# Kernel tuning notes

Measured on AMD Instinct MI355X. Metric: run time of the kernel, lower is better.

Reference implementation:

```python
import jax, jax.numpy as jnp
import numpy as np

PI = 3.14159265358979323846
MARGIN = 6.0
DIM = 256
ENT_TOT = 43234
REL_RANGE = (6.0 + 2.0) / DIM  # (margin + epsilon) / dim = 0.03125


def setup_inputs() -> dict:
    key = jax.random.key(0)
    k1, k2, k3 = jax.random.split(key, 3)
    head = jax.random.normal(k1, (32, 2 * DIM), dtype=jnp.float32)
    relation = jax.random.normal(k2, (32, DIM), dtype=jnp.float32)
    ent_emb = jax.random.normal(k3, (ENT_TOT, 2 * DIM), dtype=jnp.float32)
    return {"head": head, "relation": relation, "ent_emb": ent_emb}


def reference(head, relation, ent_emb):
    # head: (B, 2D) -> re/im halves (B, D)
    re_h, im_h = jnp.split(head, 2, axis=-1)
    # entity table: (E, 2D) -> (E, D) each
    re_t, im_t = jnp.split(ent_emb, 2, axis=-1)
    # phase rotation from relation embedding
    phase = relation / (REL_RANGE / PI)          # (B, D)
    re_r = jnp.cos(phase)
    im_r = jnp.sin(phase)
    # complex rotation of head by relation: (B, D)
    re_rot = re_h * re_r - im_h * im_r
    im_rot = re_h * im_r + im_h * re_r
    # difference against every entity, broadcast to (B, E, D)
    re_s = re_rot[:, None, :] - re_t[None, :, :]
    im_s = im_rot[:, None, :] - im_t[None, :, :]
    # L2 norm over the complex pair, summed over D -> (B, E)
    dist = jnp.sqrt(re_s * re_s + im_s * im_s).sum(axis=-1)
    return MARGIN - dist
```

## Files before the change

### kernel.cpp

```cpp
#include <hip/hip_runtime.h>
#include <math.h>

#define DIMH 256
#define NB   32
#define E_TOT 43234
#define TE   32
#define DK   32
#define NC   (DIMH / DK)
#define PHASE_DIV 0.009947183943243459f

typedef float v2f __attribute__((ext_vector_type(2)));
typedef float v4f __attribute__((ext_vector_type(4)));

__global__ __launch_bounds__(256) void rot_kernel(const float* __restrict__ head,
                                                  const float* __restrict__ rel,
                                                  float4* __restrict__ rot_v4) {
    int i  = blockIdx.x * 256 + threadIdx.x;
    int b  = i >> 7;
    int dp = i & 127;
    int d0 = dp * 2;
    float4 w;
    {
        float re_h = head[b * 2 * DIMH + d0];
        float im_h = head[b * 2 * DIMH + DIMH + d0];
        float s, c;
        sincosf(rel[b * DIMH + d0] / PHASE_DIV, &s, &c);
        w.x = re_h * c - im_h * s;
        w.z = re_h * s + im_h * c;
    }
    {
        float re_h = head[b * 2 * DIMH + d0 + 1];
        float im_h = head[b * 2 * DIMH + DIMH + d0 + 1];
        float s, c;
        sincosf(rel[b * DIMH + d0 + 1] / PHASE_DIV, &s, &c);
        w.y = re_h * c - im_h * s;
        w.w = re_h * s + im_h * c;
    }
    rot_v4[b * (DIMH / 2) + dp] = w;
}

__device__ __forceinline__ v2f sqrt2(v2f s) {
    v2f r;
    r.x = __builtin_amdgcn_sqrtf(s.x);
    r.y = __builtin_amdgcn_sqrtf(s.y);
    return r;
}

__global__ __launch_bounds__(256, 6) void dist_kernel(const float* __restrict__ ent,
                                                      const float4* __restrict__ rot_v4,
                                                      float* __restrict__ out) {
    __shared__ v4f s_e[TE][DK / 2 + 1];
    __shared__ v4f s_r[NB][DK / 2 + 1];

    const int tid = threadIdx.x;
    const int eb  = blockIdx.x * TE;
    const int ep  = tid & 15;
    const int bp  = tid >> 4;

    const int srow = tid >> 3;
    const int c4   = tid & 7;
    const int er   = min(eb + srow, E_TOT - 1);
    const int rrow = tid >> 4;
    const int rdp  = tid & 15;

    float4 p_re, p_im, p_r0, p_r1;

    auto load_chunk = [&](int c) {
        const int dk = c * DK;
        const float* b0 = &ent[(size_t)er * (2 * DIMH)];
        p_re = *reinterpret_cast<const float4*>(b0 + dk + 4 * c4);
        p_im = *reinterpret_cast<const float4*>(b0 + DIMH + dk + 4 * c4);
        p_r0 = rot_v4[rrow * (DIMH / 2) + c * (DK / 2) + rdp];
        p_r1 = rot_v4[(rrow + 16) * (DIMH / 2) + c * (DK / 2) + rdp];
    };

    v2f acc[2][2];
    #pragma unroll
    for (int j = 0; j < 2; ++j)
        #pragma unroll
        for (int k = 0; k < 2; ++k) { acc[j][k].x = 0.f; acc[j][k].y = 0.f; }

    load_chunk(0);

    for (int c = 0; c < NC; ++c) {
        {
            v4f lo, hi;
            lo.x = p_re.x; lo.y = p_re.y; lo.z = p_im.x; lo.w = p_im.y;
            hi.x = p_re.z; hi.y = p_re.w; hi.z = p_im.z; hi.w = p_im.w;
            s_e[srow][2 * c4]     = lo;
            s_e[srow][2 * c4 + 1] = hi;
            v4f r0, r1;
            r0.x = p_r0.x; r0.y = p_r0.y; r0.z = p_r0.z; r0.w = p_r0.w;
            r1.x = p_r1.x; r1.y = p_r1.y; r1.z = p_r1.z; r1.w = p_r1.w;
            s_r[rrow][rdp]      = r0;
            s_r[rrow + 16][rdp] = r1;
        }
        __syncthreads();

        if (c + 1 < NC) load_chunk(c + 1);

        #pragma unroll 4
        for (int p = 0; p < DK / 2; ++p) {
            v4f r0 = s_r[2 * bp][p];
            v4f r1 = s_r[2 * bp + 1][p];
            v4f e0 = s_e[ep][p];
            v4f e1 = s_e[ep + 16][p];

            {   v2f a = r0.xy - e0.xy, b = r0.zw - e0.zw;
                acc[0][0] += sqrt2(a * a + b * b); }
            {   v2f a = r0.xy - e1.xy, b = r0.zw - e1.zw;
                acc[0][1] += sqrt2(a * a + b * b); }
            {   v2f a = r1.xy - e0.xy, b = r1.zw - e0.zw;
                acc[1][0] += sqrt2(a * a + b * b); }
            {   v2f a = r1.xy - e1.xy, b = r1.zw - e1.zw;
                acc[1][1] += sqrt2(a * a + b * b); }
        }
        __syncthreads();
    }

    #pragma unroll
    for (int k = 0; k < 2; ++k) {
        int e = eb + ep + 16 * k;
        if (e < E_TOT) {
            #pragma unroll
            for (int j = 0; j < 2; ++j)
                out[(size_t)(2 * bp + j) * E_TOT + e] = 6.0f - (acc[j][k].x + acc[j][k].y);
        }
    }
}

extern "C" void kernel_launch(void* const* d_in, const int* in_sizes, int n_in,
                              void* d_out, int out_size, void* d_ws, size_t ws_size,
                              hipStream_t stream) {
    const float* head = (const float*)d_in[0];
    const float* rel  = (const float*)d_in[1];
    const float* ent  = (const float*)d_in[2];
    float4* rot_v4 = (float4*)d_ws;

    rot_kernel<<<(NB * DIMH / 2) / 256, 256, 0, stream>>>(head, rel, rot_v4);

    int etiles = (E_TOT + TE - 1) / TE;
    dist_kernel<<<etiles, 256, 0, stream>>>(ent, rot_v4, (float*)d_out);
}
```

Before: 173.5 us.

## Use single-wave blocks with 4x4 register tiles, swizzled LDS, and hardware sin/cos

The distance kernel moves from 256-thread blocks computing 2x2 outputs per thread to 64-thread single-wavefront blocks computing 4x4 (batch x entity) outputs per thread. This raises reuse of each LDS read and lets the __syncthreads barriers be dropped, since the whole block is one wave. XOR swizzling replaces row padding to avoid LDS bank conflicts, and output writes become float2 vector stores. The rotation kernel replaces sincosf with fractional-revolution hardware sin/cos. The trade-off is far fewer waves per CU across the same grid, which weakens latency hiding, plus lower sin/cos accuracy.

```diff
diff --git a/kernel.cpp b/kernel.cpp
--- a/kernel.cpp
+++ b/kernel.cpp
@@ -7,15 +7,14 @@
 #define TE   32
 #define DK   32
 #define NC   (DIMH / DK)
-#define PHASE_DIV 0.009947183943243459f
 
 typedef float v2f __attribute__((ext_vector_type(2)));
 typedef float v4f __attribute__((ext_vector_type(4)));
 
-__global__ __launch_bounds__(256) void rot_kernel(const float* __restrict__ head,
-                                                  const float* __restrict__ rel,
-                                                  float4* __restrict__ rot_v4) {
-    int i  = blockIdx.x * 256 + threadIdx.x;
+__global__ __launch_bounds__(64) void rot_kernel(const float* __restrict__ head,
+                                                 const float* __restrict__ rel,
+                                                 float4* __restrict__ rot_v4) {
+    int i  = blockIdx.x * 64 + threadIdx.x;
     int b  = i >> 7;
     int dp = i & 127;
     int d0 = dp * 2;
@@ -23,16 +22,20 @@
     {
         float re_h = head[b * 2 * DIMH + d0];
         float im_h = head[b * 2 * DIMH + DIMH + d0];
-        float s, c;
-        sincosf(rel[b * DIMH + d0] / PHASE_DIV, &s, &c);
+        float x = rel[b * DIMH + d0] * 16.0f;
+        float f = x - floorf(x);
+        float s = __builtin_amdgcn_sinf(f);
+        float c = __builtin_amdgcn_cosf(f);
         w.x = re_h * c - im_h * s;
         w.z = re_h * s + im_h * c;
     }
     {
         float re_h = head[b * 2 * DIMH + d0 + 1];
         float im_h = head[b * 2 * DIMH + DIMH + d0 + 1];
-        float s, c;
-        sincosf(rel[b * DIMH + d0 + 1] / PHASE_DIV, &s, &c);
+        float x = rel[b * DIMH + d0 + 1] * 16.0f;
+        float f = x - floorf(x);
+        float s = __builtin_amdgcn_sinf(f);
+        float c = __builtin_amdgcn_cosf(f);
         w.y = re_h * c - im_h * s;
         w.w = re_h * s + im_h * c;
     }
@@ -46,85 +49,111 @@
     return r;
 }
 
-__global__ __launch_bounds__(256, 6) void dist_kernel(const float* __restrict__ ent,
-                                                      const float4* __restrict__ rot_v4,
-                                                      float* __restrict__ out) {
-    __shared__ v4f s_e[TE][DK / 2 + 1];
-    __shared__ v4f s_r[NB][DK / 2 + 1];
+__global__ __launch_bounds__(64, 2) void dist_kernel(const float* __restrict__ ent,
+                                                     const float4* __restrict__ rot_v4,
+                                                     float* __restrict__ out) {
+    __shared__ v4f s_e[TE][16];
+    __shared__ v4f s_r[NB][16];
 
     const int tid = threadIdx.x;
     const int eb  = blockIdx.x * TE;
-    const int ep  = tid & 15;
-    const int bp  = tid >> 4;
+    const int eg  = tid & 7;
+    const int bg  = tid >> 3;
 
-    const int srow = tid >> 3;
-    const int c4   = tid & 7;
-    const int er   = min(eb + srow, E_TOT - 1);
+    const int erow = tid >> 3;
+    const int eq   = tid & 7;
     const int rrow = tid >> 4;
-    const int rdp  = tid & 15;
+    const int rcol = tid & 15;
 
-    float4 p_re, p_im, p_r0, p_r1;
+    float4 pe_re[4], pe_im[4], pr[8];
 
     auto load_chunk = [&](int c) {
         const int dk = c * DK;
-        const float* b0 = &ent[(size_t)er * (2 * DIMH)];
-        p_re = *reinterpret_cast<const float4*>(b0 + dk + 4 * c4);
-        p_im = *reinterpret_cast<const float4*>(b0 + DIMH + dk + 4 * c4);
-        p_r0 = rot_v4[rrow * (DIMH / 2) + c * (DK / 2) + rdp];
-        p_r1 = rot_v4[(rrow + 16) * (DIMH / 2) + c * (DK / 2) + rdp];
+        #pragma unroll
+        for (int k = 0; k < 4; ++k) {
+            int er = min(eb + 8 * k + erow, E_TOT - 1);
+            const float* b0 = ent + (size_t)er * (2 * DIMH);
+            pe_re[k] = *reinterpret_cast<const float4*>(b0 + dk + 4 * eq);
+            pe_im[k] = *reinterpret_cast<const float4*>(b0 + DIMH + dk + 4 * eq);
+        }
+        #pragma unroll
+        for (int k = 0; k < 8; ++k)
+            pr[k] = rot_v4[(4 * k + rrow) * (DIMH / 2) + c * (DK / 2) + rcol];
     };
 
-    v2f acc[2][2];
+    auto store_chunk = [&]() {
+        #pragma unroll
+        for (int k = 0; k < 4; ++k) {
+            int row = 8 * k + erow;
+            int s = (row >> 2) & 7;
+            v4f lo, hi;
+            lo.x = pe_re[k].x; lo.y = pe_re[k].y; lo.z = pe_im[k].x; lo.w = pe_im[k].y;
+            hi.x = pe_re[k].z; hi.y = pe_re[k].w; hi.z = pe_im[k].z; hi.w = pe_im[k].w;
+            s_e[row][(2 * eq)     ^ s] = lo;
+            s_e[row][(2 * eq + 1) ^ s] = hi;
+        }
+        #pragma unroll
+        for (int k = 0; k < 8; ++k) {
+            int row = 4 * k + rrow;
+            int s = (row >> 2) & 7;
+            v4f r; r.x = pr[k].x; r.y = pr[k].y; r.z = pr[k].z; r.w = pr[k].w;
+            s_r[row][rcol ^ s] = r;
+        }
+    };
+
+    v2f acc[4][4];
     #pragma unroll
-    for (int j = 0; j < 2; ++j)
+    for (int j = 0; j < 4; ++j)
         #pragma unroll
-        for (int k = 0; k < 2; ++k) { acc[j][k].x = 0.f; acc[j][k].y = 0.f; }
+        for (int k = 0; k < 4; ++k) { acc[j][k].x = 0.f; acc[j][k].y = 0.f; }
 
     load_chunk(0);
 
+    #pragma unroll 1
     for (int c = 0; c < NC; ++c) {
-        {
-            v4f lo, hi;
-            lo.x = p_re.x; lo.y = p_re.y; lo.z = p_im.x; lo.w = p_im.y;
-            hi.x = p_re.z; hi.y = p_re.w; hi.z = p_im.z; hi.w = p_im.w;
-            s_e[srow][2 * c4]     = lo;
-            s_e[srow][2 * c4 + 1] = hi;
-            v4f r0, r1;
-            r0.x = p_r0.x; r0.y = p_r0.y; r0.z = p_r0.z; r0.w = p_r0.w;
-            r1.x = p_r1.x; r1.y = p_r1.y; r1.z = p_r1.z; r1.w = p_r1.w;
-            s_r[rrow][rdp]      = r0;
-            s_r[rrow + 16][rdp] = r1;
-        }
-        __syncthreads();
-
+        store_chunk();
         if (c + 1 < NC) load_chunk(c + 1);
 
         #pragma unroll 4
         for (int p = 0; p < DK / 2; ++p) {
-            v4f r0 = s_r[2 * bp][p];
-            v4f r1 = s_r[2 * bp + 1][p];
-            v4f e0 = s_e[ep][p];
-            v4f e1 = s_e[ep + 16][p];
-
-            {   v2f a = r0.xy - e0.xy, b = r0.zw - e0.zw;
-                acc[0][0] += sqrt2(a * a + b * b); }
-            {   v2f a = r0.xy - e1.xy, b = r0.zw - e1.zw;
-                acc[0][1] += sqrt2(a * a + b * b); }
-            {   v2f a = r1.xy - e0.xy, b = r1.zw - e0.zw;
-                acc[1][0] += sqrt2(a * a + b * b); }
-            {   v2f a = r1.xy - e1.xy, b = r1.zw - e1.zw;
-                acc[1][1] += sqrt2(a * a + b * b); }
+            v4f r0 = s_r[4 * bg + 0][p ^ bg];
+            v4f r1 = s_r[4 * bg + 1][p ^ bg];
+            v4f r2 = s_r[4 * bg + 2][p ^ bg];
+            v4f r3 = s_r[4 * bg + 3][p ^ bg];
+            v4f e0 = s_e[4 * eg + 0][p ^ eg];
+            v4f e1 = s_e[4 * eg + 1][p ^ eg];
+            v4f e2 = s_e[4 * eg + 2][p ^ eg];
+            v4f e3 = s_e[4 * eg + 3][p ^ eg];
+            #define CONTRIB(J, K, R, E)                         \
+                { v2f a = R.xy - E.xy; v2f b = R.zw - E.zw;     \
+                  acc[J][K] += sqrt2(a * a + b * b); }
+            CONTRIB(0,0,r0,e0) CONTRIB(0,1,r0,e1) CONTRIB(0,2,r0,e2) CONTRIB(0,3,r0,e3)
+            CONTRIB(1,0,r1,e0) CONTRIB(1,1,r1,e1) CONTRIB(1,2,r1,e2) CONTRIB(1,3,r1,e3)
+            CONTRIB(2,0,r2,e0) CONTRIB(2,1,r2,e1) CONTRIB(2,2,r2,e2) CONTRIB(2,3,r2,e3)
+            CONTRIB(3,0,r3,e0) CONTRIB(3,1,r3,e1) CONTRIB(3,2,r3,e2) CONTRIB(3,3,r3,e3)
+            #undef CONTRIB
         }
-        __syncthreads();
     }
 
     #pragma unroll
-    for (int k = 0; k < 2; ++k) {
-        int e = eb + ep + 16 * k;
-        if (e < E_TOT) {
-            #pragma unroll
-            for (int j = 0; j < 2; ++j)
-                out[(size_t)(2 * bp + j) * E_TOT + e] = 6.0f - (acc[j][k].x + acc[j][k].y);
+    for (int j = 0; j < 4; ++j) {
+        int b = 4 * bg + j;
+        float v0 = 6.0f - (acc[j][0].x + acc[j][0].y);
+        float v1 = 6.0f - (acc[j][1].x + acc[j][1].y);
+        float v2 = 6.0f - (acc[j][2].x + acc[j][2].y);
+        float v3 = 6.0f - (acc[j][3].x + acc[j][3].y);
+        int e4 = eb + 4 * eg;
+        float* op = out + (size_t)b * E_TOT + e4;
+        if (e4 + 3 < E_TOT) {
+            float2 w0; w0.x = v0; w0.y = v1;
+            float2 w1; w1.x = v2; w1.y = v3;
+            *reinterpret_cast<float2*>(op)     = w0;
+            *reinterpret_cast<float2*>(op + 2) = w1;
+        } else {
+            if (e4     < E_TOT) op[0] = v0;
+            if (e4 + 1 < E_TOT) op[1] = v1;
+            if (e4 + 2 < E_TOT) op[2] = v2;
+            if (e4 + 3 < E_TOT) op[3] = v3;
         }
     }
 }
@@ -137,8 +166,8 @@
     const float* ent  = (const float*)d_in[2];
     float4* rot_v4 = (float4*)d_ws;
 
-    rot_kernel<<<(NB * DIMH / 2) / 256, 256, 0, stream>>>(head, rel, rot_v4);
+    rot_kernel<<<(NB * DIMH / 2) / 64, 64, 0, stream>>>(head, rel, rot_v4);
 
     int etiles = (E_TOT + TE - 1) / TE;
-    dist_kernel<<<etiles, 256, 0, stream>>>(ent, rot_v4, (float*)d_out);
+    dist_kernel<<<etiles, 64, 0, stream>>>(ent, rot_v4, (float*)d_out);
 }
```

Measured after the change: 195.7 us. 12.8% more time.
